# Kernel tuning notes

Hardware: AMD Instinct MI355X
Metric: run time of the kernel (lower is better)

Reference implementation:

```python
import jax, jax.numpy as jnp
import numpy as np

B, S, D = 8, 1024, 1024
H = 16
HD = D // H  # 64
FF = 4 * D   # 4096
EPS = 1e-5


def layer_norm(x, g, b):
    mu = jnp.mean(x, axis=-1, keepdims=True)
    var = jnp.mean(jnp.square(x - mu), axis=-1, keepdims=True)
    return (x - mu) * jax.lax.rsqrt(var + EPS) * g + b


def setup_inputs() -> dict:
    key = jax.random.key(0)
    ks = jax.random.split(key, 16)
    s_in = 1.0 / np.sqrt(D)
    s_ff = 1.0 / np.sqrt(FF)
    return {
        "x": jax.random.normal(ks[0], (B, S, D), jnp.float32),
        "ln1_g": jnp.ones((D,), jnp.float32),
        "ln1_b": jnp.zeros((D,), jnp.float32),
        "ln2_g": jnp.ones((D,), jnp.float32),
        "ln2_b": jnp.zeros((D,), jnp.float32),
        # per-head projections stacked on a leading head axis: [H, D, HD]
        "Wq": jax.random.uniform(ks[1], (H, D, HD), jnp.float32, -s_in, s_in),
        "bq": jax.random.uniform(ks[2], (H, HD), jnp.float32, -s_in, s_in),
        "Wk": jax.random.uniform(ks[3], (H, D, HD), jnp.float32, -s_in, s_in),
        "bk": jax.random.uniform(ks[4], (H, HD), jnp.float32, -s_in, s_in),
        "Wv": jax.random.uniform(ks[5], (H, D, HD), jnp.float32, -s_in, s_in),
        "bv": jax.random.uniform(ks[6], (H, HD), jnp.float32, -s_in, s_in),
        "Wo": jax.random.uniform(ks[7], (D, D), jnp.float32, -s_in, s_in),
        "bo": jax.random.uniform(ks[8], (D,), jnp.float32, -s_in, s_in),
        "W1": jax.random.uniform(ks[9], (D, FF), jnp.float32, -s_in, s_in),
        "b1": jax.random.uniform(ks[10], (FF,), jnp.float32, -s_in, s_in),
        "W2": jax.random.uniform(ks[11], (FF, D), jnp.float32, -s_ff, s_ff),
        "b2": jax.random.uniform(ks[12], (D,), jnp.float32, -s_ff, s_ff),
    }


def attention(h, Wq, bq, Wk, bk, Wv, bv, Wo, bo):
    # h: [B,S,D] -> q/k/v: [B,H,S,HD]
    q = jnp.einsum("bsd,hdk->bhsk", h, Wq) + bq[None, :, None, :]
    k = jnp.einsum("bsd,hdk->bhsk", h, Wk) + bk[None, :, None, :]
    v = jnp.einsum("bsd,hdk->bhsk", h, Wv) + bv[None, :, None, :]
    scores = jnp.einsum("bhsk,bhtk->bhst", q, k) / jnp.sqrt(jnp.float32(HD))
    w = jax.nn.softmax(scores, axis=-1)  # [B,H,S,S]
    o = jnp.einsum("bhst,bhtk->bhsk", w, v)
    # concat heads (head order matches torch.cat over per-head outputs)
    o = o.transpose(0, 2, 1, 3).reshape(h.shape[0], h.shape[1], D)
    return o @ Wo + bo


def reference(x, ln1_g, ln1_b, ln2_g, ln2_b, Wq, bq, Wk, bk, Wv, bv, Wo, bo, W1, b1, W2, b2):
    h = layer_norm(x, ln1_g, ln1_b)
    x = x + attention(h, Wq, bq, Wk, bk, Wv, bv, Wo, bo)
    h2 = layer_norm(x, ln2_g, ln2_b)
    ff = jax.nn.gelu(h2 @ W1 + b1, approximate=False) @ W2 + b2  # dropout in eval = identity
    return x + ff
```

## Files before the change

kernel.cpp:

```cpp
#include <hip/hip_runtime.h>
#include <hip/hip_bf16.h>
#include <math.h>

#define DMODEL 1024
#define NH     16
#define HD     64
#define FFDIM  4096
#define SEQ    1024
#define BATCH  8
#define ROWS   (BATCH * SEQ)

typedef __bf16 bf16x8 __attribute__((ext_vector_type(8)));
typedef __bf16 bf16x4 __attribute__((ext_vector_type(4)));
typedef float  f32x4  __attribute__((ext_vector_type(4)));

__device__ __forceinline__ unsigned short f2bf(float f) {
  unsigned int u = __builtin_bit_cast(unsigned int, f);
  u += 0x7fff + ((u >> 16) & 1);
  return (unsigned short)(u >> 16);
}

__device__ __forceinline__ void gload_lds16(const void* g, void* l) {
  __builtin_amdgcn_global_load_lds(
      (const __attribute__((address_space(1))) unsigned int*)g,
      (__attribute__((address_space(3))) unsigned int*)l, 16, 0, 0);
}

__device__ __forceinline__ bf16x8 tr_read8(const unsigned short* p) {
  bf16x4 lo, hi;
  const __attribute__((address_space(3))) unsigned short* p3 =
      (const __attribute__((address_space(3))) unsigned short*)p;
  asm volatile("ds_read_b64_tr_b16 %0, %2\n\t"
               "ds_read_b64_tr_b16 %1, %2 offset:128"
               : "=v"(lo), "=v"(hi)
               : "v"(p3));
  return __builtin_shufflevector(lo, hi, 0, 1, 2, 3, 4, 5, 6, 7);
}

__global__ __launch_bounds__(256) void ln_bf16_kernel(
    const float* __restrict__ x, const float* __restrict__ g,
    const float* __restrict__ bta, unsigned short* __restrict__ out) {
  int row = blockIdx.x;
  int tid = threadIdx.x;
  int wid = tid >> 6, lane = tid & 63;
  const float4 v = ((const float4*)(x + (size_t)row * DMODEL))[tid];
  float s = v.x + v.y + v.z + v.w;
#pragma unroll
  for (int off = 32; off >= 1; off >>= 1) s += __shfl_xor(s, off, 64);
  __shared__ float red[8];
  if (lane == 0) red[wid] = s;
  __syncthreads();
  float mu = (red[0] + red[1] + red[2] + red[3]) * (1.0f / DMODEL);
  float4 d;
  d.x = v.x - mu; d.y = v.y - mu; d.z = v.z - mu; d.w = v.w - mu;
  float sq = d.x * d.x + d.y * d.y + d.z * d.z + d.w * d.w;
#pragma unroll
  for (int off = 32; off >= 1; off >>= 1) sq += __shfl_xor(sq, off, 64);
  if (lane == 0) red[4 + wid] = sq;
  __syncthreads();
  float var = (red[4] + red[5] + red[6] + red[7]) * (1.0f / DMODEL);
  float rs = rsqrtf(var + 1e-5f);
  const float4 gg = ((const float4*)g)[tid];
  const float4 bb = ((const float4*)bta)[tid];
  ushort4 o;
  o.x = f2bf(d.x * rs * gg.x + bb.x);
  o.y = f2bf(d.y * rs * gg.y + bb.y);
  o.z = f2bf(d.z * rs * gg.z + bb.z);
  o.w = f2bf(d.w * rs * gg.w + bb.w);
  ((ushort4*)(out + (size_t)row * DMODEL))[tid] = o;
}

__global__ __launch_bounds__(256) void transpose_f2b_kernel(
    const float* __restrict__ in, unsigned short* __restrict__ out,
    int R, int C, long long ibs, long long obs) {
  __shared__ float tile[64][65];
  int b = blockIdx.z;
  int r0 = blockIdx.y * 64, c0 = blockIdx.x * 64;
  const float* ip = in + (size_t)b * ibs;
  unsigned short* op = out + (size_t)b * obs;
  int tid = threadIdx.x;
  int rl = tid >> 4, cl = (tid & 15) * 4;
#pragma unroll
  for (int it = 0; it < 4; ++it) {
    int r = it * 16 + rl;
    float4 v = *(const float4*)(ip + (size_t)(r0 + r) * C + c0 + cl);
    tile[r][cl] = v.x; tile[r][cl + 1] = v.y;
    tile[r][cl + 2] = v.z; tile[r][cl + 3] = v.w;
  }
  __syncthreads();
#pragma unroll
  for (int it = 0; it < 4; ++it) {
    int c = it * 16 + rl;
    ushort4 o;
    o.x = f2bf(tile[cl + 0][c]); o.y = f2bf(tile[cl + 1][c]);
    o.z = f2bf(tile[cl + 2][c]); o.w = f2bf(tile[cl + 3][c]);
    *(ushort4*)(op + (size_t)(c0 + c) * R + r0 + cl) = o;
  }
}

__global__ __launch_bounds__(256) void transpose_v_kernel(
    const unsigned short* __restrict__ V, unsigned short* __restrict__ Vt) {
  __shared__ unsigned short tile[64][68];
  int bh = blockIdx.y;
  int b = bh >> 4, h = bh & 15;
  int t0 = blockIdx.x * 64;
  int tid = threadIdx.x;
  int rl = tid >> 4, cl = (tid & 15) * 4;
  const unsigned short* ip = V + ((size_t)(b * SEQ + t0)) * DMODEL + h * HD;
#pragma unroll
  for (int it = 0; it < 4; ++it) {
    int t = it * 16 + rl;
    ushort4 v = *(const ushort4*)(ip + (size_t)t * DMODEL + cl);
    tile[t][cl] = v.x; tile[t][cl + 1] = v.y;
    tile[t][cl + 2] = v.z; tile[t][cl + 3] = v.w;
  }
  __syncthreads();
  unsigned short* op = Vt + ((size_t)bh * HD) * SEQ + t0;
#pragma unroll
  for (int it = 0; it < 4; ++it) {
    int d = it * 16 + rl;
    ushort4 o;
    o.x = tile[cl + 0][d]; o.y = tile[cl + 1][d];
    o.z = tile[cl + 2][d]; o.w = tile[cl + 3][d];
    *(ushort4*)(op + (size_t)d * SEQ + cl) = o;
  }
}

#define QSCALE 0.18033688f

template <int EPI>
__global__ __launch_bounds__(512, 4) void gemmdb_kernel(
    const unsigned short* __restrict__ A, const unsigned short* __restrict__ Bt,
    const float* __restrict__ bias, const float* __restrict__ bias2,
    const float* __restrict__ bias3, const float* __restrict__ resid,
    unsigned short* __restrict__ outb, unsigned short* __restrict__ outb2,
    unsigned short* __restrict__ outb3, float* __restrict__ outf,
    int M, int N, int K, int NX) {
  __shared__ __align__(16) unsigned short As[2 * 128 * 64];
  __shared__ __align__(16) unsigned short Bs[2 * 128 * 64];

  const int tid = threadIdx.x;
  const int wid = tid >> 6, lane = tid & 63;
  const int l15 = lane & 15, l4 = lane >> 4;
  const int wm = wid >> 1, wn = wid & 1;

  const int cpx = (int)gridDim.x >> 3;
  const int swz = ((int)blockIdx.x & 7) * cpx + ((int)blockIdx.x >> 3);
  const int by = swz / NX, bx = swz % NX;

  const size_t KBY = (size_t)K * 2;

  const int rS = tid >> 3;
  const int cS = ((tid & 7) ^ (rS & 7)) << 4;
  const char* gA = (const char*)A + (size_t)(by * 128 + rS) * KBY + cS;
  const char* gB = (const char*)Bt + (size_t)(bx * 128 + rS) * KBY + cS;
  char* sA = (char*)As + tid * 16;
  char* sB = (char*)Bs + tid * 16;

  const int rsw = (l4 ^ (l15 & 7)) << 4;
  const char* aRd0 = (const char*)As + (wm * 32 + l15) * 128 + rsw;
  const char* aRd1 = (const char*)As + (wm * 32 + l15) * 128 + (rsw ^ 64);
  const char* bRd0 = (const char*)Bs + (wn * 64 + l15) * 128 + rsw;
  const char* bRd1 = (const char*)Bs + (wn * 64 + l15) * 128 + (rsw ^ 64);

  f32x4 acc[2][4];
  const f32x4 fz = {0.f, 0.f, 0.f, 0.f};
#pragma unroll
  for (int i = 0; i < 2; ++i)
#pragma unroll
    for (int j = 0; j < 4; ++j) acc[i][j] = fz;

  const int nt = K >> 6;

  gload_lds16(gA, sA);
  gload_lds16(gA + 64 * KBY, sA + 8192);
  gload_lds16(gB, sB);
  gload_lds16(gB + 64 * KBY, sB + 8192);
  asm volatile("s_waitcnt vmcnt(0)" ::: "memory");
  __builtin_amdgcn_sched_barrier(0);
  __builtin_amdgcn_s_barrier();
  __builtin_amdgcn_sched_barrier(0);

#pragma unroll 1
  for (int t = 0; t < nt; ++t) {
    const int cur = t & 1;
    if (t + 1 < nt) {
      const size_t ko = (size_t)(t + 1) << 7;
      const int nb = (cur ^ 1) << 14;
      gload_lds16(gA + ko, sA + nb);
      gload_lds16(gA + 64 * KBY + ko, sA + nb + 8192);
      gload_lds16(gB + ko, sB + nb);
      gload_lds16(gB + 64 * KBY + ko, sB + nb + 8192);
    }
    const int off = cur << 14;
#pragma unroll
    for (int kk = 0; kk < 2; ++kk) {
      const char* aR = (kk ? aRd1 : aRd0) + off;
      const char* bR = (kk ? bRd1 : bRd0) + off;
      bf16x8 afr[2], bfr[4];
#pragma unroll
      for (int ni = 0; ni < 4; ++ni) bfr[ni] = *(const bf16x8*)(bR + ni * 2048);
#pragma unroll
      for (int mi = 0; mi < 2; ++mi) afr[mi] = *(const bf16x8*)(aR + mi * 2048);
      __builtin_amdgcn_s_setprio(1);
#pragma unroll
      for (int mi = 0; mi < 2; ++mi)
#pragma unroll
        for (int ni = 0; ni < 4; ++ni)
          acc[mi][ni] = __builtin_amdgcn_mfma_f32_16x16x32_bf16(
              afr[mi], bfr[ni], acc[mi][ni], 0, 0, 0);
      __builtin_amdgcn_s_setprio(0);
    }
    asm volatile("s_waitcnt vmcnt(0)" ::: "memory");
    __builtin_amdgcn_sched_barrier(0);
    __builtin_amdgcn_s_barrier();
    __builtin_amdgcn_sched_barrier(0);
  }

  if (EPI == 5) {
    const int range = bx >> 3;
    const float* bp = (range == 0) ? bias : (range == 1) ? bias2 : bias3;
    unsigned short* op = (range == 0) ? outb : (range == 1) ? outb2 : outb3;
    const float scale = (range == 0) ? QSCALE : 1.0f;
#pragma unroll
    for (int mi = 0; mi < 2; ++mi) {
#pragma unroll
      for (int ni = 0; ni < 4; ++ni) {
        int colL = (bx & 7) * 128 + wn * 64 + ni * 16 + l15;
        float bn = bp[colL];
#pragma unroll
        for (int jj = 0; jj < 4; ++jj) {
          int row = by * 128 + wm * 32 + mi * 16 + l4 * 4 + jj;
          op[(size_t)row * 1024 + colL] = f2bf((acc[mi][ni][jj] + bn) * scale);
        }
      }
    }
  } else {
#pragma unroll
    for (int mi = 0; mi < 2; ++mi) {
#pragma unroll
      for (int ni = 0; ni < 4; ++ni) {
        int col = bx * 128 + wn * 64 + ni * 16 + l15;
        float bn = bias[col];
#pragma unroll
        for (int jj = 0; jj < 4; ++jj) {
          int row = by * 128 + wm * 32 + mi * 16 + l4 * 4 + jj;
          float v = acc[mi][ni][jj] + bn;
          if (EPI == 1 || EPI == 3) {
            outf[(size_t)row * N + col] = v + resid[(size_t)row * N + col];
          } else if (EPI == 2) {
            float gel = 0.5f * v * (1.0f + erff(v * 0.70710678118f));
            outb[(size_t)row * N + col] = f2bf(gel);
          } else {
            outb[(size_t)row * N + col] = f2bf(v);
          }
        }
      }
    }
  }
}

__global__ __launch_bounds__(256, 3) void attn_kernel(
    const unsigned short* __restrict__ Q, const unsigned short* __restrict__ K,
    const unsigned short* __restrict__ Vt, unsigned short* __restrict__ O) {
  __shared__ __align__(16) unsigned short Ks[128 * 64];
  __shared__ __align__(16) unsigned short Vs[64 * 128];
  __shared__ __align__(16) unsigned short Ps[4][128 * 16];
  int tid = threadIdx.x, wid = tid >> 6, lane = tid & 63;
  int l15 = lane & 15, l4 = lane >> 4;
  int sid = blockIdx.x;
  int aid = (sid & 7) * 256 + (sid >> 3);
  int bh = aid >> 4, qb = aid & 15;
  int b = bh >> 4, h = bh & 15;
  int q0 = qb * 64 + wid * 16;
  const f32x4 fz = {0.f, 0.f, 0.f, 0.f};

  const unsigned short* Qbase = Q + ((size_t)(b * SEQ + q0)) * DMODEL + h * HD;
  bf16x8 qf[2];
#pragma unroll
  for (int kh = 0; kh < 2; ++kh)
    qf[kh] = *(const bf16x8*)(Qbase + (size_t)l15 * DMODEL + kh * 32 + l4 * 8);

  f32x4 o[4];
#pragma unroll
  for (int i = 0; i < 4; ++i) o[i] = fz;
  float mrun[4], lrun[4];
#pragma unroll
  for (int j = 0; j < 4; ++j) { mrun[j] = -1e30f; lrun[j] = 0.0f; }

  const unsigned short* Kb = K + (size_t)b * SEQ * DMODEL + h * HD;
  const unsigned short* Vb = Vt + (size_t)bh * HD * SEQ;
  unsigned short* pbase = &Ps[wid][0];
  int krow = tid >> 3, kchunk = tid & 7;
  int vrow = tid >> 4, vchunk = tid & 15;

  for (int t0 = 0; t0 < SEQ; t0 += 128) {
    __syncthreads();
#pragma unroll
    for (int p = 0; p < 4; ++p) {
      int kr = p * 32 + krow;
      int kg = kchunk ^ (kr & 7);
      gload_lds16(Kb + (size_t)(t0 + kr) * DMODEL + kg * 8,
                  (char*)Ks + p * 4096 + tid * 16);
      int vr = p * 16 + vrow;
      int vg = vchunk ^ (vr & 7);
      gload_lds16(Vb + (size_t)vr * SEQ + t0 + vg * 8,
                  (char*)Vs + p * 4096 + tid * 16);
    }
    __syncthreads();
    f32x4 s[8];
#pragma unroll
    for (int ts = 0; ts < 8; ++ts) {
      int row = ts * 16 + l15;
      bf16x8 k0f = *(const bf16x8*)((const char*)Ks + row * 128 + ((l4) ^ (row & 7)) * 16);
      bf16x8 k1f = *(const bf16x8*)((const char*)Ks + row * 128 + ((4 + l4) ^ (row & 7)) * 16);
      s[ts] = __builtin_amdgcn_mfma_f32_16x16x32_bf16(qf[0], k0f, fz, 0, 0, 0);
      s[ts] = __builtin_amdgcn_mfma_f32_16x16x32_bf16(qf[1], k1f, s[ts], 0, 0, 0);
    }
#pragma unroll
    for (int j = 0; j < 4; ++j) {
      float tm = fmaxf(fmaxf(fmaxf(s[0][j], s[1][j]), fmaxf(s[2][j], s[3][j])),
                       fmaxf(fmaxf(s[4][j], s[5][j]), fmaxf(s[6][j], s[7][j])));
#pragma unroll
      for (int off = 8; off >= 1; off >>= 1) tm = fmaxf(tm, __shfl_xor(tm, off, 16));
      float mnew = fmaxf(mrun[j], tm);
      float alpha = __builtin_amdgcn_exp2f(mrun[j] - mnew);
      float ps = 0.0f;
#pragma unroll
      for (int ts = 0; ts < 8; ++ts) {
        float p = __builtin_amdgcn_exp2f(s[ts][j] - mnew);
        s[ts][j] = p;
        ps += p;
      }
#pragma unroll
      for (int off = 8; off >= 1; off >>= 1) ps += __shfl_xor(ps, off, 16);
      lrun[j] = lrun[j] * alpha + ps;
      mrun[j] = mnew;
#pragma unroll
      for (int d = 0; d < 4; ++d) o[d][j] *= alpha;
    }
#pragma unroll
    for (int ts = 0; ts < 8; ++ts) {
      ushort4 pk;
      pk.x = f2bf(s[ts][0]); pk.y = f2bf(s[ts][1]);
      pk.z = f2bf(s[ts][2]); pk.w = f2bf(s[ts][3]);
      *(ushort4*)((char*)pbase + (ts * 16 + l15) * 32 + l4 * 8) = pk;
    }
    asm volatile("s_waitcnt lgkmcnt(0)" ::: "memory");
    __builtin_amdgcn_sched_barrier(0);
#pragma unroll
    for (int kp = 0; kp < 4; ++kp) {
      bf16x8 pf = tr_read8(pbase + (kp * 32 + l4 * 8) * 16 + l15);
      asm volatile("s_waitcnt lgkmcnt(0)" ::: "memory");
      __builtin_amdgcn_sched_barrier(0);
#pragma unroll
      for (int d = 0; d < 4; ++d) {
        int vr = d * 16 + l15;
        int vphys = (kp * 4 + l4) ^ (vr & 7);
        bf16x8 vf = *(const bf16x8*)((const char*)Vs + vr * 256 + vphys * 16);
        o[d] = __builtin_amdgcn_mfma_f32_16x16x32_bf16(pf, vf, o[d], 0, 0, 0);
      }
    }
  }
  unsigned short* Ob = O + ((size_t)(b * SEQ + q0)) * DMODEL + h * HD;
#pragma unroll
  for (int j = 0; j < 4; ++j) {
    float inv = 1.0f / lrun[j];
#pragma unroll
    for (int d = 0; d < 4; ++d) {
      int row = l4 * 4 + j;
      Ob[(size_t)row * DMODEL + d * 16 + l15] = f2bf(o[d][j] * inv);
    }
  }
}

extern "C" void kernel_launch(void* const* d_in, const int* in_sizes, int n_in,
                              void* d_out, int out_size, void* d_ws, size_t ws_size,
                              hipStream_t stream) {
  (void)in_sizes; (void)n_in; (void)out_size; (void)ws_size;
  const float* x    = (const float*)d_in[0];
  const float* ln1g = (const float*)d_in[1];
  const float* ln1b = (const float*)d_in[2];
  const float* ln2g = (const float*)d_in[3];
  const float* ln2b = (const float*)d_in[4];
  const float* Wq   = (const float*)d_in[5];
  const float* bq   = (const float*)d_in[6];
  const float* Wk   = (const float*)d_in[7];
  const float* bk   = (const float*)d_in[8];
  const float* Wv   = (const float*)d_in[9];
  const float* bv   = (const float*)d_in[10];
  const float* Wo   = (const float*)d_in[11];
  const float* bo   = (const float*)d_in[12];
  const float* W1   = (const float*)d_in[13];
  const float* b1   = (const float*)d_in[14];
  const float* W2   = (const float*)d_in[15];
  const float* b2   = (const float*)d_in[16];
  float* out = (float*)d_out;

  char* ws = (char*)d_ws;
  const size_t MB = 1u << 20;
  unsigned short* wqT = (unsigned short*)(ws + 0 * MB);
  unsigned short* wkT = (unsigned short*)(ws + 2 * MB);
  unsigned short* wvT = (unsigned short*)(ws + 4 * MB);
  unsigned short* woT = (unsigned short*)(ws + 6 * MB);
  unsigned short* w1T = (unsigned short*)(ws + 8 * MB);
  unsigned short* w2T = (unsigned short*)(ws + 16 * MB);
  unsigned short* hb  = (unsigned short*)(ws + 24 * MB);
  unsigned short* Qb  = (unsigned short*)(ws + 40 * MB);
  unsigned short* Kb  = (unsigned short*)(ws + 56 * MB);
  unsigned short* Vb  = (unsigned short*)(ws + 72 * MB);
  unsigned short* Vt  = (unsigned short*)(ws + 88 * MB);
  unsigned short* Ob  = Vb;
  unsigned short* ff1 = (unsigned short*)(ws + 40 * MB);

  transpose_f2b_kernel<<<dim3(1, 16, 16), 256, 0, stream>>>(Wq, wqT, 1024, 64,
                                                            65536LL, 65536LL);
  transpose_f2b_kernel<<<dim3(1, 16, 16), 256, 0, stream>>>(Wk, wkT, 1024, 64,
                                                            65536LL, 65536LL);
  transpose_f2b_kernel<<<dim3(1, 16, 16), 256, 0, stream>>>(Wv, wvT, 1024, 64,
                                                            65536LL, 65536LL);
  transpose_f2b_kernel<<<dim3(16, 16, 1), 256, 0, stream>>>(Wo, woT, 1024, 1024, 0, 0);
  transpose_f2b_kernel<<<dim3(64, 16, 1), 256, 0, stream>>>(W1, w1T, 1024, 4096, 0, 0);
  transpose_f2b_kernel<<<dim3(16, 64, 1), 256, 0, stream>>>(W2, w2T, 4096, 1024, 0, 0);

  ln_bf16_kernel<<<dim3(ROWS), 256, 0, stream>>>(x, ln1g, ln1b, hb);

  gemmdb_kernel<5><<<dim3(1536), 512, 0, stream>>>(
      hb, wqT, bq, bk, bv, nullptr, Qb, Kb, Vb, nullptr, ROWS, 1024, DMODEL, 24);

  transpose_v_kernel<<<dim3(16, 128), 256, 0, stream>>>(Vb, Vt);

  attn_kernel<<<dim3(2048), 256, 0, stream>>>(Qb, Kb, Vt, Ob);

  gemmdb_kernel<1><<<dim3(512), 512, 0, stream>>>(
      Ob, woT, bo, nullptr, nullptr, x, nullptr, nullptr, nullptr, out,
      ROWS, DMODEL, DMODEL, 8);

  ln_bf16_kernel<<<dim3(ROWS), 256, 0, stream>>>(out, ln2g, ln2b, hb);

  gemmdb_kernel<2><<<dim3(2048), 512, 0, stream>>>(
      hb, w1T, b1, nullptr, nullptr, nullptr, ff1, nullptr, nullptr, nullptr,
      ROWS, FFDIM, DMODEL, 32);

  gemmdb_kernel<3><<<dim3(512), 512, 0, stream>>>(
      ff1, w2T, b2, nullptr, nullptr, out, nullptr, nullptr, nullptr, out,
      ROWS, DMODEL, FFDIM, 8);
}
```

Before: 403.6 us.

## Rewrite GEMM with 256-row tiles and 4-stage K=32 async LDS pipeline

Replaces the 128x128 double-buffered GEMM with a 256xBN tile (BN 128 or 256), split into K=32 slices held in a 4-slot LDS ring with partial vmcnt waits. Three loads stay in flight while MFMA runs on the current slice. Each wave now holds up to 8x4 accumulators, and occupancy drops to 2 blocks per CU. Block swizzling changes to a fixed grouping of 4 row-blocks, and grid sizes shrink to match. The larger tiles raise operand reuse and the deeper prefetch hides global latency, at the cost of more registers, fewer waves and fewer blocks for the small GEMMs.

```diff
diff --git a/kernel.cpp b/kernel.cpp
--- a/kernel.cpp
+++ b/kernel.cpp
@@ -35,6 +35,21 @@
                : "=v"(lo), "=v"(hi)
                : "v"(p3));
   return __builtin_shufflevector(lo, hi, 0, 1, 2, 3, 4, 5, 6, 7);
+}
+
+template <int N>
+__device__ __forceinline__ void wait_vm() {
+  if constexpr (N == 0)
+    asm volatile("s_waitcnt vmcnt(0)" ::: "memory");
+  else if constexpr (N == 3)
+    asm volatile("s_waitcnt vmcnt(3)" ::: "memory");
+  else if constexpr (N == 4)
+    asm volatile("s_waitcnt vmcnt(4)" ::: "memory");
+  else if constexpr (N == 6)
+    asm volatile("s_waitcnt vmcnt(6)" ::: "memory");
+  else
+    asm volatile("s_waitcnt vmcnt(8)" ::: "memory");
+  __builtin_amdgcn_sched_barrier(0);
 }
 
 __global__ __launch_bounds__(256) void ln_bf16_kernel(
@@ -128,94 +143,97 @@
 
 #define QSCALE 0.18033688f
 
-template <int EPI>
-__global__ __launch_bounds__(512, 4) void gemmdb_kernel(
+template <int BN, int EPI>
+__global__ __launch_bounds__(512, 2) void gemma_kernel(
     const unsigned short* __restrict__ A, const unsigned short* __restrict__ Bt,
     const float* __restrict__ bias, const float* __restrict__ bias2,
     const float* __restrict__ bias3, const float* __restrict__ resid,
     unsigned short* __restrict__ outb, unsigned short* __restrict__ outb2,
     unsigned short* __restrict__ outb3, float* __restrict__ outf,
-    int M, int N, int K, int NX) {
-  __shared__ __align__(16) unsigned short As[2 * 128 * 64];
-  __shared__ __align__(16) unsigned short Bs[2 * 128 * 64];
+    int M, int N, int K) {
+  constexpr int MREP = (BN == 256) ? 8 : 4;
+  constexpr int WM = MREP * 16;
+  constexpr int NW = BN / 64;
+  constexpr int LPT = (BN == 256) ? 4 : 3;
+  constexpr int BSZB = BN * 64;
+  __shared__ __align__(16) unsigned short As[4 * 256 * 32];
+  __shared__ __align__(16) unsigned short Bs[4 * BN * 32];
 
   const int tid = threadIdx.x;
   const int wid = tid >> 6, lane = tid & 63;
   const int l15 = lane & 15, l4 = lane >> 4;
-  const int wm = wid >> 1, wn = wid & 1;
-
-  const int cpx = (int)gridDim.x >> 3;
-  const int swz = ((int)blockIdx.x & 7) * cpx + ((int)blockIdx.x >> 3);
-  const int by = swz / NX, bx = swz % NX;
+  const int wm = wid / NW, wn = wid % NW;
+
+  const int id = (int)blockIdx.x;
+  const int i = id >> 3;
+  const int by = (id & 7) * 4 + (i & 3);
+  const int bx = i >> 2;
 
   const size_t KBY = (size_t)K * 2;
 
-  const int rS = tid >> 3;
-  const int cS = ((tid & 7) ^ (rS & 7)) << 4;
-  const char* gA = (const char*)A + (size_t)(by * 128 + rS) * KBY + cS;
-  const char* gB = (const char*)Bt + (size_t)(bx * 128 + rS) * KBY + cS;
+  const int rS = tid >> 2;
+  const int cS = (((tid & 3) ^ ((tid >> 3) & 3))) << 4;
+  const char* gA0 = (const char*)A + (size_t)(by * 256 + rS) * KBY + cS;
+  const char* gA1 = gA0 + 128 * KBY;
+  const char* gB0 = (const char*)Bt + (size_t)(bx * BN + rS) * KBY + cS;
+  const char* gB1 = gB0 + 128 * KBY;
   char* sA = (char*)As + tid * 16;
   char* sB = (char*)Bs + tid * 16;
 
-  const int rsw = (l4 ^ (l15 & 7)) << 4;
-  const char* aRd0 = (const char*)As + (wm * 32 + l15) * 128 + rsw;
-  const char* aRd1 = (const char*)As + (wm * 32 + l15) * 128 + (rsw ^ 64);
-  const char* bRd0 = (const char*)Bs + (wn * 64 + l15) * 128 + rsw;
-  const char* bRd1 = (const char*)Bs + (wn * 64 + l15) * 128 + (rsw ^ 64);
-
-  f32x4 acc[2][4];
+  const int fsw = (l4 ^ ((l15 >> 1) & 3)) << 4;
+  const char* aRd = (const char*)As + (wm * WM + l15) * 64 + fsw;
+  const char* bRd = (const char*)Bs + (wn * 64 + l15) * 64 + fsw;
+
+  f32x4 acc[MREP][4];
   const f32x4 fz = {0.f, 0.f, 0.f, 0.f};
 #pragma unroll
-  for (int i = 0; i < 2; ++i)
-#pragma unroll
-    for (int j = 0; j < 4; ++j) acc[i][j] = fz;
-
-  const int nt = K >> 6;
-
-  gload_lds16(gA, sA);
-  gload_lds16(gA + 64 * KBY, sA + 8192);
-  gload_lds16(gB, sB);
-  gload_lds16(gB + 64 * KBY, sB + 8192);
-  asm volatile("s_waitcnt vmcnt(0)" ::: "memory");
-  __builtin_amdgcn_sched_barrier(0);
-  __builtin_amdgcn_s_barrier();
-  __builtin_amdgcn_sched_barrier(0);
+  for (int i2 = 0; i2 < MREP; ++i2)
+#pragma unroll
+    for (int j = 0; j < 4; ++j) acc[i2][j] = fz;
+
+  const int nt = K >> 5;
+
+#define STAGE(SLOT, T)                                                       \
+  do {                                                                       \
+    const size_t ko_ = (size_t)(T) * 64;                                     \
+    gload_lds16(gA0 + ko_, sA + (SLOT) * 16384);                             \
+    gload_lds16(gA1 + ko_, sA + (SLOT) * 16384 + 8192);                      \
+    gload_lds16(gB0 + ko_, sB + (SLOT) * BSZB);                              \
+    if constexpr (BN == 256) gload_lds16(gB1 + ko_, sB + (SLOT) * BSZB + 8192); \
+  } while (0)
+
+#define TILE(T, VMN, PF)                                                     \
+  do {                                                                       \
+    wait_vm<(VMN)>();                                                        \
+    __builtin_amdgcn_s_barrier();                                            \
+    __builtin_amdgcn_sched_barrier(0);                                       \
+    if (PF) STAGE(((T) + 3) & 3, (T) + 3);                                   \
+    {                                                                        \
+      const char* aB = aRd + ((T) & 3) * 16384;                              \
+      const char* bB = bRd + ((T) & 3) * BSZB;                               \
+      bf16x8 av[MREP], bv[4];                                                \
+      _Pragma("unroll") for (int ni = 0; ni < 4; ++ni)                       \
+          bv[ni] = *(const bf16x8*)(bB + ni * 1024);                         \
+      _Pragma("unroll") for (int mi = 0; mi < MREP; ++mi)                    \
+          av[mi] = *(const bf16x8*)(aB + mi * 1024);                         \
+      __builtin_amdgcn_s_setprio(1);                                         \
+      _Pragma("unroll") for (int mi = 0; mi < MREP; ++mi)                    \
+          _Pragma("unroll") for (int ni = 0; ni < 4; ++ni)                   \
+              acc[mi][ni] = __builtin_amdgcn_mfma_f32_16x16x32_bf16(         \
+                  av[mi], bv[ni], acc[mi][ni], 0, 0, 0);                     \
+      __builtin_amdgcn_s_setprio(0);                                         \
+    }                                                                        \
+  } while (0)
+
+  STAGE(0, 0);
+  STAGE(1, 1);
+  STAGE(2, 2);
 
 #pragma unroll 1
-  for (int t = 0; t < nt; ++t) {
-    const int cur = t & 1;
-    if (t + 1 < nt) {
-      const size_t ko = (size_t)(t + 1) << 7;
-      const int nb = (cur ^ 1) << 14;
-      gload_lds16(gA + ko, sA + nb);
-      gload_lds16(gA + 64 * KBY + ko, sA + nb + 8192);
-      gload_lds16(gB + ko, sB + nb);
-      gload_lds16(gB + 64 * KBY + ko, sB + nb + 8192);
-    }
-    const int off = cur << 14;
-#pragma unroll
-    for (int kk = 0; kk < 2; ++kk) {
-      const char* aR = (kk ? aRd1 : aRd0) + off;
-      const char* bR = (kk ? bRd1 : bRd0) + off;
-      bf16x8 afr[2], bfr[4];
-#pragma unroll
-      for (int ni = 0; ni < 4; ++ni) bfr[ni] = *(const bf16x8*)(bR + ni * 2048);
-#pragma unroll
-      for (int mi = 0; mi < 2; ++mi) afr[mi] = *(const bf16x8*)(aR + mi * 2048);
-      __builtin_amdgcn_s_setprio(1);
-#pragma unroll
-      for (int mi = 0; mi < 2; ++mi)
-#pragma unroll
-        for (int ni = 0; ni < 4; ++ni)
-          acc[mi][ni] = __builtin_amdgcn_mfma_f32_16x16x32_bf16(
-              afr[mi], bfr[ni], acc[mi][ni], 0, 0, 0);
-      __builtin_amdgcn_s_setprio(0);
-    }
-    asm volatile("s_waitcnt vmcnt(0)" ::: "memory");
-    __builtin_amdgcn_sched_barrier(0);
-    __builtin_amdgcn_s_barrier();
-    __builtin_amdgcn_sched_barrier(0);
-  }
+  for (int t = 0; t < nt - 3; ++t) TILE(t, 2 * LPT, 1);
+  TILE(nt - 3, 2 * LPT, 0);
+  TILE(nt - 2, LPT, 0);
+  TILE(nt - 1, 0, 0);
 
   if (EPI == 5) {
     const int range = bx >> 3;
@@ -223,30 +241,30 @@
     unsigned short* op = (range == 0) ? outb : (range == 1) ? outb2 : outb3;
     const float scale = (range == 0) ? QSCALE : 1.0f;
 #pragma unroll
-    for (int mi = 0; mi < 2; ++mi) {
+    for (int mi = 0; mi < MREP; ++mi) {
 #pragma unroll
       for (int ni = 0; ni < 4; ++ni) {
         int colL = (bx & 7) * 128 + wn * 64 + ni * 16 + l15;
         float bn = bp[colL];
 #pragma unroll
         for (int jj = 0; jj < 4; ++jj) {
-          int row = by * 128 + wm * 32 + mi * 16 + l4 * 4 + jj;
+          int row = by * 256 + wm * WM + mi * 16 + l4 * 4 + jj;
           op[(size_t)row * 1024 + colL] = f2bf((acc[mi][ni][jj] + bn) * scale);
         }
       }
     }
   } else {
 #pragma unroll
-    for (int mi = 0; mi < 2; ++mi) {
+    for (int mi = 0; mi < MREP; ++mi) {
 #pragma unroll
       for (int ni = 0; ni < 4; ++ni) {
-        int col = bx * 128 + wn * 64 + ni * 16 + l15;
+        int col = bx * BN + wn * 64 + ni * 16 + l15;
         float bn = bias[col];
 #pragma unroll
         for (int jj = 0; jj < 4; ++jj) {
-          int row = by * 128 + wm * 32 + mi * 16 + l4 * 4 + jj;
+          int row = by * 256 + wm * WM + mi * 16 + l4 * 4 + jj;
           float v = acc[mi][ni][jj] + bn;
-          if (EPI == 1 || EPI == 3) {
+          if (EPI == 1) {
             outf[(size_t)row * N + col] = v + resid[(size_t)row * N + col];
           } else if (EPI == 2) {
             float gel = 0.5f * v * (1.0f + erff(v * 0.70710678118f));
@@ -258,6 +276,8 @@
       }
     }
   }
+#undef STAGE
+#undef TILE
 }
 
 __global__ __launch_bounds__(256, 3) void attn_kernel(
@@ -425,24 +445,24 @@
 
   ln_bf16_kernel<<<dim3(ROWS), 256, 0, stream>>>(x, ln1g, ln1b, hb);
 
-  gemmdb_kernel<5><<<dim3(1536), 512, 0, stream>>>(
-      hb, wqT, bq, bk, bv, nullptr, Qb, Kb, Vb, nullptr, ROWS, 1024, DMODEL, 24);
+  gemma_kernel<128, 5><<<dim3(768), 512, 0, stream>>>(
+      hb, wqT, bq, bk, bv, nullptr, Qb, Kb, Vb, nullptr, ROWS, 1024, DMODEL);
 
   transpose_v_kernel<<<dim3(16, 128), 256, 0, stream>>>(Vb, Vt);
 
   attn_kernel<<<dim3(2048), 256, 0, stream>>>(Qb, Kb, Vt, Ob);
 
-  gemmdb_kernel<1><<<dim3(512), 512, 0, stream>>>(
+  gemma_kernel<128, 1><<<dim3(256), 512, 0, stream>>>(
       Ob, woT, bo, nullptr, nullptr, x, nullptr, nullptr, nullptr, out,
-      ROWS, DMODEL, DMODEL, 8);
+      ROWS, DMODEL, DMODEL);
 
   ln_bf16_kernel<<<dim3(ROWS), 256, 0, stream>>>(out, ln2g, ln2b, hb);
 
-  gemmdb_kernel<2><<<dim3(2048), 512, 0, stream>>>(
+  gemma_kernel<256, 2><<<dim3(512), 512, 0, stream>>>(
       hb, w1T, b1, nullptr, nullptr, nullptr, ff1, nullptr, nullptr, nullptr,
-      ROWS, FFDIM, DMODEL, 32);
-
-  gemmdb_kernel<3><<<dim3(512), 512, 0, stream>>>(
+      ROWS, FFDIM, DMODEL);
+
+  gemma_kernel<128, 1><<<dim3(256), 512, 0, stream>>>(
       ff1, w2T, b2, nullptr, nullptr, out, nullptr, nullptr, nullptr, out,
-      ROWS, DMODEL, FFDIM, 8);
-}
+      ROWS, DMODEL, FFDIM);
+}
```

New measurement: 464.5 us. 15.1% more time.
